# Kernel tuning notes

Hardware: AMD Instinct MI355X
Metric: run time of the kernel (lower is better)

Reference implementation:

```python
import jax, jax.numpy as jnp
import numpy as np

EMBED = 1024
HEADS = 16
HEAD_DIM = EMBED // HEADS


def setup_inputs() -> dict:
    key = jax.random.key(0)
    ks = jax.random.split(key, 6)
    s = 1.0 / np.sqrt(EMBED)
    return {
        "x": jax.random.normal(ks[0], (2, 2048, EMBED), dtype=jnp.float32),
        "Wq": jax.random.normal(ks[1], (EMBED, EMBED), dtype=jnp.float32) * s,
        "Wk": jax.random.normal(ks[2], (EMBED, EMBED), dtype=jnp.float32) * s,
        "Wv": jax.random.normal(ks[3], (EMBED, EMBED), dtype=jnp.float32) * s,
        "Wfc": jax.random.normal(ks[4], (EMBED, EMBED), dtype=jnp.float32) * s,
        "bfc": jnp.zeros((EMBED,), dtype=jnp.float32),
    }


def reference(x, Wq, Wk, Wv, Wfc, bfc):
    # x: (N, L, E). Linear(E,E,bias=False) applies y = x @ W.T (torch convention).
    N, L, E = x.shape
    q = (x @ Wq.T).reshape(N, L, HEADS, HEAD_DIM)
    k = (x @ Wk.T).reshape(N, L, HEADS, HEAD_DIM)
    v = (x @ Wv.T).reshape(N, L, HEADS, HEAD_DIM)
    # energy: (N, H, Q, K)
    energy = jnp.einsum('nqhd,nkhd->nhqk', q, k)
    # NOTE: original scales by sqrt(embed_size), not sqrt(head_dim)
    attn = jax.nn.softmax(energy / jnp.sqrt(jnp.float32(E)), axis=3)
    out = jnp.einsum('nhql,nlhd->nqhd', attn, v).reshape(N, L, E)
    return out @ Wfc.T + bfc
```

## Files before the change

### kernel.cpp

```cpp
#include <hip/hip_runtime.h>
#include <stdint.h>


typedef short bf16x8 __attribute__((ext_vector_type(8)));
typedef short bf16x4 __attribute__((ext_vector_type(4)));
typedef float f32x4 __attribute__((ext_vector_type(4)));

__device__ __forceinline__ unsigned short f2bf(float f) {
  union { float f; unsigned u; } v; v.f = f;
  return (unsigned short)((v.u + 0x7FFFu + ((v.u >> 16) & 1u)) >> 16);
}

#if defined(__has_builtin)
#if __has_builtin(__builtin_amdgcn_cvt_pk_bf16_f32)
#define HAVE_PK_BF16 1
#endif
#if __has_builtin(__builtin_amdgcn_exp2f)
#define EXP2(x) __builtin_amdgcn_exp2f(x)
#endif
#endif
#ifndef EXP2
#define EXP2(x) exp2f(x)
#endif

__device__ __forceinline__ unsigned pk2bf(float a, float b) {
#ifdef HAVE_PK_BF16
  typedef __bf16 bfv2 __attribute__((ext_vector_type(2)));
  union { bfv2 v; unsigned u; } c;
  c.v = __builtin_amdgcn_cvt_pk_bf16_f32(a, b);
  return c.u;
#else
  return (unsigned)f2bf(a) | ((unsigned)f2bf(b) << 16);
#endif
}

__device__ __forceinline__ void load_lds16(const unsigned short* g, unsigned short* l) {
  __builtin_amdgcn_global_load_lds(
      (const __attribute__((address_space(1))) unsigned int*)(const void*)g,
      (__attribute__((address_space(3))) unsigned int*)(void*)l, 16, 0, 0);
}

#define MFMA16(a, b, c) __builtin_amdgcn_mfma_f32_16x16x32_bf16((a), (b), (c), 0, 0, 0)

#if defined(__has_builtin)
#if __has_builtin(__builtin_amdgcn_mfma_f32_16x16x16bf16_1k)
#define MFMAK16(a, b, c) __builtin_amdgcn_mfma_f32_16x16x16bf16_1k((a), (b), (c), 0, 0, 0)
#elif __has_builtin(__builtin_amdgcn_mfma_f32_16x16x16_bf16)
#define MFMAK16(a, b, c) __builtin_amdgcn_mfma_f32_16x16x16_bf16((a), (b), (c), 0, 0, 0)
#endif
#endif
#ifndef MFMAK16
__device__ __forceinline__ f32x4 mfmak16_asm(bf16x4 a, bf16x4 b, f32x4 c) {
  asm volatile("v_mfma_f32_16x16x16_bf16 %0, %1, %2, %0" : "+v"(c) : "v"(a), "v"(b));
  return c;
}
#define MFMAK16(a, b, c) mfmak16_asm((a), (b), (c))
#endif

__global__ __launch_bounds__(256) void cvt_all_kernel(
    const float* __restrict__ x, const float* __restrict__ w0, const float* __restrict__ w1,
    const float* __restrict__ w2, const float* __restrict__ w3, unsigned short* __restrict__ xb,
    unsigned short* __restrict__ d0, unsigned short* __restrict__ d1,
    unsigned short* __restrict__ d2, unsigned short* __restrict__ d3) {
  int i = blockIdx.x * 256 + threadIdx.x;
  const float* s;
  unsigned short* d;
  int off;
  if (i < 1048576) {
    s = x; d = xb; off = i;
  } else {
    int j = i - 1048576;
    int w = j >> 18;
    off = j & 262143;
    s = (w == 0) ? w0 : (w == 1) ? w1 : (w == 2) ? w2 : w3;
    d = (w == 0) ? d0 : (w == 1) ? d1 : (w == 2) ? d2 : d3;
  }
  float4 f = ((const float4*)s)[off];
  uint2 o;
  o.x = pk2bf(f.x, f.y);
  o.y = pk2bf(f.z, f.w);
  ((uint2*)d)[off] = o;
}

__global__ __launch_bounds__(256) void gemm_qkv_kernel(
    const unsigned short* __restrict__ Xb, const unsigned short* __restrict__ Wqb,
    const unsigned short* __restrict__ Wkb, const unsigned short* __restrict__ Wvb,
    unsigned short* __restrict__ Qo, unsigned short* __restrict__ Ko,
    unsigned short* __restrict__ Vt) {
  __shared__ __align__(16) unsigned short As[128 * 32];
  __shared__ __align__(16) unsigned short Bs[128 * 32];
  const int mode = blockIdx.z;
  const unsigned short* W = (mode == 0) ? Wqb : ((mode == 1) ? Wkb : Wvb);
  const int n0 = blockIdx.x * 128;
  const int m0 = blockIdx.y * 128;
  const int tid = threadIdx.x;
  const int lane = tid & 63;
  const int wv = tid >> 6;
  const int wm = (wv >> 1) * 64;
  const int wn = (wv & 1) * 64;
  const int qq = lane >> 4;
  const int cc = lane & 15;

  const f32x4 fz = {0.f, 0.f, 0.f, 0.f};
  f32x4 acc[4][4];
#pragma unroll
  for (int i = 0; i < 4; i++)
#pragma unroll
    for (int j = 0; j < 4; j++) acc[i][j] = fz;

  const int ia0 = tid, ia1 = tid + 256;
  const int ra0 = ia0 >> 2, ca0 = (ia0 & 3) * 8;
  const int ra1 = ia1 >> 2, ca1 = (ia1 & 3) * 8;

  for (int k0 = 0; k0 < 1024; k0 += 32) {
    __syncthreads();
    load_lds16(Xb + (m0 + ra0) * 1024 + k0 + ca0, As + ia0 * 8);
    load_lds16(Xb + (m0 + ra1) * 1024 + k0 + ca1, As + ia1 * 8);
    load_lds16(W + (n0 + ra0) * 1024 + k0 + ca0, Bs + ia0 * 8);
    load_lds16(W + (n0 + ra1) * 1024 + k0 + ca1, Bs + ia1 * 8);
    __syncthreads();
    bf16x8 a[4], b[4];
#pragma unroll
    for (int i = 0; i < 4; i++) a[i] = *(const bf16x8*)(As + (wm + i * 16 + cc) * 32 + qq * 8);
#pragma unroll
    for (int j = 0; j < 4; j++) b[j] = *(const bf16x8*)(Bs + (wn + j * 16 + cc) * 32 + qq * 8);
    if (mode < 2) {
#pragma unroll
      for (int i = 0; i < 4; i++)
#pragma unroll
        for (int j = 0; j < 4; j++) acc[i][j] = MFMA16(b[j], a[i], acc[i][j]);
    } else {
#pragma unroll
      for (int i = 0; i < 4; i++)
#pragma unroll
        for (int j = 0; j < 4; j++) acc[i][j] = MFMA16(a[i], b[j], acc[i][j]);
    }
  }

  if (mode < 2) {
    const float esc = (mode == 0) ? 0.0450842200277801f : 1.0f;
    unsigned short* dst = (mode == 0) ? Qo : Ko;
#pragma unroll
    for (int i = 0; i < 4; i++) {
      int row = m0 + wm + i * 16 + cc;
#pragma unroll
      for (int j = 0; j < 4; j++) {
        int col = n0 + wn + j * 16 + qq * 4;
        uint2 pk;
        pk.x = pk2bf(acc[i][j][0] * esc, acc[i][j][1] * esc);
        pk.y = pk2bf(acc[i][j][2] * esc, acc[i][j][3] * esc);
        *(uint2*)(dst + row * 1024 + col) = pk;
      }
    }
  } else {
#pragma unroll
    for (int i = 0; i < 4; i++)
#pragma unroll
      for (int j = 0; j < 4; j++) {
        int row = m0 + wm + i * 16 + qq * 4;
        int nn = row >> 11, ll = row & 2047;
        int col = n0 + wn + j * 16 + cc;
        int hh = col >> 6, dd = col & 63;
        uint2 pk;
        pk.x = pk2bf(acc[i][j][0], acc[i][j][1]);
        pk.y = pk2bf(acc[i][j][2], acc[i][j][3]);
        *(uint2*)(Vt + ((nn * 16 + hh) * 64 + dd) * 2048 + ll) = pk;
      }
  }
}

__global__ __launch_bounds__(128, 1) void attn_kernel(const unsigned short* __restrict__ Qg,
                                                      const unsigned short* __restrict__ Kg,
                                                      const unsigned short* __restrict__ Vg,
                                                      unsigned short* __restrict__ Og) {
  __shared__ __align__(16) unsigned short Kl[2][128 * 64];
  __shared__ __align__(16) unsigned short Vl[2][64 * 128];
  const int qt = blockIdx.x, hh = blockIdx.y, nb = blockIdx.z;
  const int tid = threadIdx.x, lane = tid & 63, wv = tid >> 6;
  const int qq = lane >> 4, cc = lane & 15;
  const int q0 = qt * 128 + wv * 64;
  const unsigned short* Kbase = Kg + (size_t)(nb * 2048) * 1024 + hh * 64;
  const unsigned short* Vbase = Vg + (size_t)((nb * 16 + hh) * 64) * 2048;

  const int cK = tid & 7, rKb = tid >> 3;
  const int swK = ((cK ^ (rKb & 7)) << 3);
  const int cV = tid & 15, rVb = tid >> 4;

  bf16x8 qf[4][2];
#pragma unroll
  for (int rt = 0; rt < 4; rt++)
#pragma unroll
    for (int kc = 0; kc < 2; kc++)
      qf[rt][kc] = *(const bf16x8*)(Qg + (size_t)(nb * 2048 + q0 + rt * 16 + cc) * 1024 +
                                    hh * 64 + kc * 32 + qq * 8);

  const f32x4 fz = {0.f, 0.f, 0.f, 0.f};
  const bf16x4 onesA = {(short)0x3F80, (short)0x3F80, (short)0x3F80, (short)0x3F80};
  f32x4 o[4][4];
  f32x4 lacc[4];
#pragma unroll
  for (int rt = 0; rt < 4; rt++) {
    lacc[rt] = fz;
#pragma unroll
    for (int vt = 0; vt < 4; vt++) o[rt][vt] = fz;
  }

  bf16x8 kbuf[8], vbuf[8];
#pragma unroll
  for (int p = 0; p < 8; p++)
    kbuf[p] = *(const bf16x8*)(Kbase + (size_t)(p * 16 + rKb) * 1024 + cK * 8);
#pragma unroll
  for (int p = 0; p < 8; p++)
    vbuf[p] = *(const bf16x8*)(Vbase + (size_t)(p * 8 + rVb) * 2048 + cV * 8);
#pragma unroll
  for (int p = 0; p < 8; p++) *(bf16x8*)(Kl[0] + (p * 16 + rKb) * 64 + swK) = kbuf[p];
#pragma unroll
  for (int p = 0; p < 8; p++)
    *(bf16x8*)(Vl[0] + (p * 8 + rVb) * 128 + ((cV ^ (((p & 1) << 3) | rVb)) << 3)) = vbuf[p];
  __syncthreads();

#pragma unroll 1
  for (int it = 0; it < 16; it++) {
    const int cur = it & 1;
    const unsigned short* Kc = Kl[cur];
    const unsigned short* Vc = Vl[cur];
    if (it < 15) {
      const size_t ktn = (size_t)(it + 1) * 128;
#pragma unroll
      for (int p = 0; p < 8; p++)
        kbuf[p] = *(const bf16x8*)(Kbase + (ktn + p * 16 + rKb) * 1024 + cK * 8);
#pragma unroll
      for (int p = 0; p < 8; p++)
        vbuf[p] = *(const bf16x8*)(Vbase + (size_t)(p * 8 + rVb) * 2048 + ktn + cV * 8);
    }
#pragma unroll
    for (int st = 0; st < 8; st++) {
      const unsigned short* kr = Kc + (st * 16 + cc) * 64;
      int ch0 = (qq ^ (cc & 7)) << 3;
      bf16x8 k0 = *(const bf16x8*)(kr + ch0);
      bf16x8 k1 = *(const bf16x8*)(kr + (ch0 ^ 32));
      f32x4 z[4];
#pragma unroll
      for (int rt = 0; rt < 4; rt++) {
        z[rt] = MFMA16(k0, qf[rt][0], fz);
        z[rt] = MFMA16(k1, qf[rt][1], z[rt]);
      }
      bf16x4 bp[4];
#pragma unroll
      for (int rt = 0; rt < 4; rt++) {
        float p0 = EXP2(z[rt][0]), p1 = EXP2(z[rt][1]);
        float p2 = EXP2(z[rt][2]), p3 = EXP2(z[rt][3]);
        union { uint2 u; bf16x4 v; } pk;
        pk.u.x = pk2bf(p0, p1);
        pk.u.y = pk2bf(p2, p3);
        bp[rt] = pk.v;
        lacc[rt] = MFMAK16(onesA, bp[rt], lacc[rt]);
      }
      int vc = st * 2 + (qq >> 1);
      int voff = (qq & 1) * 4;
#pragma unroll
      for (int vt = 0; vt < 4; vt++) {
        bf16x4 vf = *(const bf16x4*)(Vc + (vt * 16 + cc) * 128 + ((vc ^ cc) << 3) + voff);
#pragma unroll
        for (int rt = 0; rt < 4; rt++) o[rt][vt] = MFMAK16(vf, bp[rt], o[rt][vt]);
      }
    }
    if (it < 15) {
      unsigned short* Kn = Kl[cur ^ 1];
      unsigned short* Vn = Vl[cur ^ 1];
#pragma unroll
      for (int p = 0; p < 8; p++) *(bf16x8*)(Kn + (p * 16 + rKb) * 64 + swK) = kbuf[p];
#pragma unroll
      for (int p = 0; p < 8; p++)
        *(bf16x8*)(Vn + (p * 8 + rVb) * 128 + ((cV ^ (((p & 1) << 3) | rVb)) << 3)) = vbuf[p];
    }
    __syncthreads();
  }

#pragma unroll
  for (int rt = 0; rt < 4; rt++) {
    float rinv = 1.0f / lacc[rt][0];
#pragma unroll
    for (int vt = 0; vt < 4; vt++) {
      uint2 ov;
      ov.x = pk2bf(o[rt][vt][0] * rinv, o[rt][vt][1] * rinv);
      ov.y = pk2bf(o[rt][vt][2] * rinv, o[rt][vt][3] * rinv);
      *(uint2*)(Og + (size_t)(nb * 2048 + q0 + rt * 16 + cc) * 1024 + hh * 64 + vt * 16 +
                qq * 4) = ov;
    }
  }
}

__global__ __launch_bounds__(256) void gemm_fc_kernel(const unsigned short* __restrict__ Ab,
                                                      const unsigned short* __restrict__ Wb,
                                                      const float* __restrict__ bias,
                                                      float* __restrict__ Co) {
  __shared__ __align__(16) unsigned short As[64 * 32];
  __shared__ __align__(16) unsigned short Bs[128 * 32];
  const int n0 = blockIdx.x * 128;
  const int m0 = blockIdx.y * 64;
  const int tid = threadIdx.x;
  const int lane = tid & 63;
  const int wv = tid >> 6;
  const int wm = (wv & 1) * 32;
  const int wn = (wv >> 1) * 64;
  const int qq = lane >> 4;
  const int cc = lane & 15;

  const f32x4 fz = {0.f, 0.f, 0.f, 0.f};
  f32x4 acc[2][4];
#pragma unroll
  for (int i = 0; i < 2; i++)
#pragma unroll
    for (int j = 0; j < 4; j++) acc[i][j] = fz;

  const int raA = tid >> 2, caA = (tid & 3) * 8;
  const int ia0 = tid, ia1 = tid + 256;
  const int rb0 = ia0 >> 2, cb0 = (ia0 & 3) * 8;
  const int rb1 = ia1 >> 2, cb1 = (ia1 & 3) * 8;

  for (int k0 = 0; k0 < 1024; k0 += 32) {
    __syncthreads();
    load_lds16(Ab + (m0 + raA) * 1024 + k0 + caA, As + tid * 8);
    load_lds16(Wb + (n0 + rb0) * 1024 + k0 + cb0, Bs + ia0 * 8);
    load_lds16(Wb + (n0 + rb1) * 1024 + k0 + cb1, Bs + ia1 * 8);
    __syncthreads();
    bf16x8 a[2], b[4];
#pragma unroll
    for (int i = 0; i < 2; i++) a[i] = *(const bf16x8*)(As + (wm + i * 16 + cc) * 32 + qq * 8);
#pragma unroll
    for (int j = 0; j < 4; j++) b[j] = *(const bf16x8*)(Bs + (wn + j * 16 + cc) * 32 + qq * 8);
#pragma unroll
    for (int i = 0; i < 2; i++)
#pragma unroll
      for (int j = 0; j < 4; j++) acc[i][j] = MFMA16(b[j], a[i], acc[i][j]);
  }

#pragma unroll
  for (int i = 0; i < 2; i++) {
    int row = m0 + wm + i * 16 + cc;
#pragma unroll
    for (int j = 0; j < 4; j++) {
      int col = n0 + wn + j * 16 + qq * 4;
      float4 bb = *(const float4*)(bias + col);
      float4 ov;
      ov.x = acc[i][j][0] + bb.x;
      ov.y = acc[i][j][1] + bb.y;
      ov.z = acc[i][j][2] + bb.z;
      ov.w = acc[i][j][3] + bb.w;
      *(float4*)(Co + (size_t)row * 1024 + col) = ov;
    }
  }
}

extern "C" void kernel_launch(void* const* d_in, const int* in_sizes, int n_in, void* d_out,
                              int out_size, void* d_ws, size_t ws_size, hipStream_t stream) {
  const float* x = (const float*)d_in[0];
  const float* Wq = (const float*)d_in[1];
  const float* Wk = (const float*)d_in[2];
  const float* Wv = (const float*)d_in[3];
  const float* Wfc = (const float*)d_in[4];
  const float* bfc = (const float*)d_in[5];
  float* out = (float*)d_out;
  char* ws = (char*)d_ws;
  unsigned short* xb = (unsigned short*)(ws);
  unsigned short* wqb = (unsigned short*)(ws + (8u << 20));
  unsigned short* wkb = (unsigned short*)(ws + (10u << 20));
  unsigned short* wvb = (unsigned short*)(ws + (12u << 20));
  unsigned short* wfb = (unsigned short*)(ws + (14u << 20));
  unsigned short* Qb = (unsigned short*)(ws + (16u << 20));
  unsigned short* Kb = (unsigned short*)(ws + (24u << 20));
  unsigned short* Vtb = (unsigned short*)(ws + (32u << 20));
  unsigned short* Ob = (unsigned short*)(ws + (40u << 20));

  cvt_all_kernel<<<8192, 256, 0, stream>>>(x, Wq, Wk, Wv, Wfc, xb, wqb, wkb, wvb, wfb);
  gemm_qkv_kernel<<<dim3(8, 32, 3), 256, 0, stream>>>(xb, wqb, wkb, wvb, Qb, Kb, Vtb);
  attn_kernel<<<dim3(16, 16, 2), 128, 0, stream>>>(Qb, Kb, Vtb, Ob);
  gemm_fc_kernel<<<dim3(8, 64), 256, 0, stream>>>(Ob, wfb, bfc, out);
}
```

Before: 225.4 us.

## Split attention key range across two wave pairs and merge partial outputs

The attention block grows from 128 to 256 threads. Two wave pairs each process half of the 2048 keys (8 tiles each) into their own shared-memory K/V buffers, then combine partial O and row sums through shared memory before normalising. This doubles the waves per block to raise occupancy and latency hiding for the 512-block grid. In exchange it drops the LDS double buffering, so global loads are now overlapped only through registers, and it adds a shared-memory reduction at the end. The merge stays exact because the kernel uses no running max.

Result: faster. 212.0 us (-6.0%).

```diff
diff --git a/kernel.cpp b/kernel.cpp
--- a/kernel.cpp
+++ b/kernel.cpp
@@ -169,22 +169,26 @@
   }
 }
 
-__global__ __launch_bounds__(128, 1) void attn_kernel(const unsigned short* __restrict__ Qg,
+__global__ __launch_bounds__(256, 2) void attn_kernel(const unsigned short* __restrict__ Qg,
                                                       const unsigned short* __restrict__ Kg,
                                                       const unsigned short* __restrict__ Vg,
                                                       unsigned short* __restrict__ Og) {
-  __shared__ __align__(16) unsigned short Kl[2][128 * 64];
-  __shared__ __align__(16) unsigned short Vl[2][64 * 128];
+  __shared__ __align__(16) unsigned short smem[2][128 * 64 + 64 * 128];
   const int qt = blockIdx.x, hh = blockIdx.y, nb = blockIdx.z;
   const int tid = threadIdx.x, lane = tid & 63, wv = tid >> 6;
+  const int pair = wv >> 1, wq = wv & 1;
+  const int ptid = tid & 127;
   const int qq = lane >> 4, cc = lane & 15;
-  const int q0 = qt * 128 + wv * 64;
-  const unsigned short* Kbase = Kg + (size_t)(nb * 2048) * 1024 + hh * 64;
-  const unsigned short* Vbase = Vg + (size_t)((nb * 16 + hh) * 64) * 2048;
-
-  const int cK = tid & 7, rKb = tid >> 3;
-  const int swK = ((cK ^ (rKb & 7)) << 3);
-  const int cV = tid & 15, rVb = tid >> 4;
+  const int q0 = qt * 128 + wq * 64;
+  const int kb = pair * 1024;
+  unsigned short* Kp = smem[pair];
+  unsigned short* Vp = smem[pair] + 128 * 64;
+  const unsigned short* Kbase = Kg + (size_t)(nb * 2048 + kb) * 1024 + hh * 64;
+  const unsigned short* Vbase = Vg + (size_t)((nb * 16 + hh) * 64) * 2048 + kb;
+
+  const int cK = ptid & 7, rKb = ptid >> 3;
+  const int swK = (cK ^ (rKb & 7)) << 3;
+  const int cV = ptid & 15, rVb = ptid >> 4;
 
   bf16x8 qf[4][2];
 #pragma unroll
@@ -212,19 +216,17 @@
 #pragma unroll
   for (int p = 0; p < 8; p++)
     vbuf[p] = *(const bf16x8*)(Vbase + (size_t)(p * 8 + rVb) * 2048 + cV * 8);
-#pragma unroll
-  for (int p = 0; p < 8; p++) *(bf16x8*)(Kl[0] + (p * 16 + rKb) * 64 + swK) = kbuf[p];
-#pragma unroll
-  for (int p = 0; p < 8; p++)
-    *(bf16x8*)(Vl[0] + (p * 8 + rVb) * 128 + ((cV ^ (((p & 1) << 3) | rVb)) << 3)) = vbuf[p];
-  __syncthreads();
 
 #pragma unroll 1
-  for (int it = 0; it < 16; it++) {
-    const int cur = it & 1;
-    const unsigned short* Kc = Kl[cur];
-    const unsigned short* Vc = Vl[cur];
-    if (it < 15) {
+  for (int it = 0; it < 8; it++) {
+    __syncthreads();
+#pragma unroll
+    for (int p = 0; p < 8; p++) *(bf16x8*)(Kp + (p * 16 + rKb) * 64 + swK) = kbuf[p];
+#pragma unroll
+    for (int p = 0; p < 8; p++)
+      *(bf16x8*)(Vp + (p * 8 + rVb) * 128 + ((cV ^ (((p & 1) << 3) | rVb)) << 3)) = vbuf[p];
+    __syncthreads();
+    if (it < 7) {
       const size_t ktn = (size_t)(it + 1) * 128;
 #pragma unroll
       for (int p = 0; p < 8; p++)
@@ -235,7 +237,7 @@
     }
 #pragma unroll
     for (int st = 0; st < 8; st++) {
-      const unsigned short* kr = Kc + (st * 16 + cc) * 64;
+      const unsigned short* kr = Kp + (st * 16 + cc) * 64;
       int ch0 = (qq ^ (cc & 7)) << 3;
       bf16x8 k0 = *(const bf16x8*)(kr + ch0);
       bf16x8 k1 = *(const bf16x8*)(kr + (ch0 ^ 32));
@@ -260,33 +262,42 @@
       int voff = (qq & 1) * 4;
 #pragma unroll
       for (int vt = 0; vt < 4; vt++) {
-        bf16x4 vf = *(const bf16x4*)(Vc + (vt * 16 + cc) * 128 + ((vc ^ cc) << 3) + voff);
+        bf16x4 vf = *(const bf16x4*)(Vp + (vt * 16 + cc) * 128 + ((vc ^ cc) << 3) + voff);
 #pragma unroll
         for (int rt = 0; rt < 4; rt++) o[rt][vt] = MFMAK16(vf, bp[rt], o[rt][vt]);
       }
     }
-    if (it < 15) {
-      unsigned short* Kn = Kl[cur ^ 1];
-      unsigned short* Vn = Vl[cur ^ 1];
-#pragma unroll
-      for (int p = 0; p < 8; p++) *(bf16x8*)(Kn + (p * 16 + rKb) * 64 + swK) = kbuf[p];
-#pragma unroll
-      for (int p = 0; p < 8; p++)
-        *(bf16x8*)(Vn + (p * 8 + rVb) * 128 + ((cV ^ (((p & 1) << 3) | rVb)) << 3)) = vbuf[p];
-    }
-    __syncthreads();
-  }
-
-#pragma unroll
-  for (int rt = 0; rt < 4; rt++) {
-    float rinv = 1.0f / lacc[rt][0];
-#pragma unroll
-    for (int vt = 0; vt < 4; vt++) {
-      uint2 ov;
-      ov.x = pk2bf(o[rt][vt][0] * rinv, o[rt][vt][1] * rinv);
-      ov.y = pk2bf(o[rt][vt][2] * rinv, o[rt][vt][3] * rinv);
-      *(uint2*)(Og + (size_t)(nb * 2048 + q0 + rt * 16 + cc) * 1024 + hh * 64 + vt * 16 +
-                qq * 4) = ov;
+  }
+
+  float* oex = (float*)&smem[0][0];
+  float* lex = oex + 8192;
+  __syncthreads();
+  if (pair == 1) {
+#pragma unroll
+    for (int rt = 0; rt < 4; rt++) {
+#pragma unroll
+      for (int vt = 0; vt < 4; vt++) {
+        int idx = (((wq * 4 + rt) * 4 + vt) * 4 + qq) * 16 + cc;
+        *(f32x4*)(oex + idx * 4) = o[rt][vt];
+      }
+      if (qq == 0) lex[(wq * 4 + rt) * 16 + cc] = lacc[rt][0];
+    }
+  }
+  __syncthreads();
+  if (pair == 0) {
+#pragma unroll
+    for (int rt = 0; rt < 4; rt++) {
+      float rinv = 1.0f / (lacc[rt][0] + lex[(wq * 4 + rt) * 16 + cc]);
+#pragma unroll
+      for (int vt = 0; vt < 4; vt++) {
+        int idx = (((wq * 4 + rt) * 4 + vt) * 4 + qq) * 16 + cc;
+        f32x4 op = *(const f32x4*)(oex + idx * 4);
+        uint2 ov;
+        ov.x = pk2bf((o[rt][vt][0] + op[0]) * rinv, (o[rt][vt][1] + op[1]) * rinv);
+        ov.y = pk2bf((o[rt][vt][2] + op[2]) * rinv, (o[rt][vt][3] + op[3]) * rinv);
+        *(uint2*)(Og + (size_t)(nb * 2048 + q0 + rt * 16 + cc) * 1024 + hh * 64 + vt * 16 +
+                  qq * 4) = ov;
+      }
     }
   }
 }
@@ -375,6 +386,6 @@
 
   cvt_all_kernel<<<8192, 256, 0, stream>>>(x, Wq, Wk, Wv, Wfc, xb, wqb, wkb, wvb, wfb);
   gemm_qkv_kernel<<<dim3(8, 32, 3), 256, 0, stream>>>(xb, wqb, wkb, wvb, Qb, Kb, Vtb);
-  attn_kernel<<<dim3(16, 16, 2), 128, 0, stream>>>(Qb, Kb, Vtb, Ob);
+  attn_kernel<<<dim3(16, 16, 2), 256, 0, stream>>>(Qb, Kb, Vtb, Ob);
   gemm_fc_kernel<<<dim3(8, 64), 256, 0, stream>>>(Ob, wfb, bfc, out);
 }
```
